# Optimization experiments

Measured on AMD Instinct MI355X. Metric: run time of the kernel, lower is better.

## Reference

```python
import jax, jax.numpy as jnp
import numpy as np

B, T, H, W, D = 8, 16, 64, 64, 256
DK = 128
TOP_K = 4
DECAY = 0.95
TAU = 1.0
EPS = 1e-10


def setup_inputs() -> dict:
    key = jax.random.key(0)
    ks = jax.random.split(key, 6)
    return {
        "query_features": jax.random.normal(ks[0], (B, H, W, D), dtype=jnp.float32),
        "history_buffer": jax.random.normal(ks[1], (B, T, H, W, D), dtype=jnp.float32),
        "W_q": jax.random.normal(ks[2], (D, DK), dtype=jnp.float32) * (1.0 / np.sqrt(D)),
        "W_k": jax.random.normal(ks[3], (D, DK), dtype=jnp.float32) * (1.0 / np.sqrt(D)),
        "W_v": jax.random.normal(ks[4], (D, DK), dtype=jnp.float32) * (1.0 / np.sqrt(D)),
        "W_o": jax.random.normal(ks[5], (DK, D), dtype=jnp.float32) * (1.0 / np.sqrt(DK)),
    }


def reference(query_features, history_buffer, W_q, W_k, W_v, W_o):
    # Projections (Linear, bias=False)
    Q = jnp.einsum("bhwd,dk->bhwk", query_features, W_q)          # [B,H,W,DK]
    K = jnp.einsum("bthwd,dk->bthwk", history_buffer, W_k)        # [B,T,H,W,DK]
    V = jnp.einsum("bthwd,dk->bthwk", history_buffer, W_v)        # [B,T,H,W,DK]

    # Per-pixel temporal scores over T history steps
    scores = jnp.einsum("bhwk,bthwk->bhwt", Q, K) / jnp.sqrt(jnp.float32(DK))  # [B,H,W,T]

    # Top-K gating over the time axis (top_k < T)
    _, topk_idx = jax.lax.top_k(scores, TOP_K)                    # [B,H,W,K]
    mask = jax.nn.one_hot(topk_idx, T, dtype=scores.dtype).sum(axis=-2) > 0  # [B,H,W,T]
    scores = jnp.where(mask, scores, -jnp.inf)

    # Log-decay bias: decay_rate ** (T - t)
    t = jnp.arange(T, dtype=jnp.float32)
    decay_bias = jnp.log(jnp.float32(DECAY) ** (T - t) + EPS)     # [T]
    scores = scores + decay_bias

    attn = jax.nn.softmax(scores / TAU, axis=-1)                  # [B,H,W,T]

    out = jnp.einsum("bhwt,bthwk->bhwk", attn, V)                 # [B,H,W,DK]
    out = jnp.einsum("bhwk,kd->bhwd", out, W_o)                   # [B,H,W,D]
    return out
```

## Files before the change

### kernel.cpp

```cpp
#include <hip/hip_runtime.h>
#include <math.h>


typedef __attribute__((ext_vector_type(8))) short bf16x8;
typedef __attribute__((ext_vector_type(4))) float f32x4;

__device__ inline unsigned short f2bf(float f) {
  union { float f; unsigned u; } v; v.f = f;
  unsigned r = (v.u + 0x7FFF + ((v.u >> 16) & 1)) >> 16;
  return (unsigned short)r;
}
__device__ inline float bf2f(unsigned short h) {
  union { unsigned u; float f; } v; v.u = ((unsigned)h) << 16;
  return v.f;
}
__device__ inline float4 ldnt(const float4* p) {
  f32x4 t = __builtin_nontemporal_load((const f32x4*)p);
  return make_float4(t[0], t[1], t[2], t[3]);
}

__global__ __launch_bounds__(256) void precompute_weights(
    const float* __restrict__ Wq, const float* __restrict__ Wk,
    const float* __restrict__ Wv, const float* __restrict__ Wo,
    unsigned short* __restrict__ M1A, unsigned short* __restrict__ M1B,
    unsigned short* __restrict__ M1C, unsigned short* __restrict__ M2F) {
  __shared__ float rowbuf[128];
  int bid = blockIdx.x, tid = threadIdx.x;
  if (bid < 256) {
    int d = bid;
    if (tid < 128) rowbuf[tid] = Wq[d * 128 + tid];
    __syncthreads();
    const float4* Wk4 = (const float4*)Wk;
    const float4* rb4 = (const float4*)rowbuf;
    float acc = 0.f;
#pragma unroll 8
    for (int k4 = 0; k4 < 32; ++k4) {
      float4 a = rb4[k4];
      float4 b = Wk4[tid * 32 + k4];
      acc = fmaf(a.x, b.x, acc); acc = fmaf(a.y, b.y, acc);
      acc = fmaf(a.z, b.z, acc); acc = fmaf(a.w, b.w, acc);
    }
    int c = tid;
    int ct = c >> 4, kt = d >> 5, lh = (d >> 3) & 3, i = d & 7, lm = c & 15;
    size_t idx = (size_t)(((ct * 8 + kt) * 64 + lh * 16 + lm) * 8 + i);
    unsigned short h0 = f2bf(acc);
    float r1 = acc - bf2f(h0);
    unsigned short h1 = f2bf(r1);
    float r2 = r1 - bf2f(h1);
    M1A[idx] = h0;
    M1B[idx] = h1;
    M1C[idx] = f2bf(r2);
  } else {
    int k = bid - 256;
    if (tid < 128) rowbuf[tid] = Wv[k * 128 + tid];
    __syncthreads();
    float acc = 0.f;
#pragma unroll 8
    for (int kk = 0; kk < 128; ++kk)
      acc = fmaf(rowbuf[kk], Wo[kk * 256 + tid], acc);
    int c = tid;
    int ct = c >> 4, kt = k >> 5, lh = (k >> 3) & 3, i = k & 7, lm = c & 15;
    M2F[(size_t)(((ct * 8 + kt) * 64 + lh * 16 + lm) * 8 + i)] = f2bf(acc);
  }
}

__global__ __launch_bounds__(256, 2) void fused_all(
    const float* __restrict__ query, const float* __restrict__ hist,
    const unsigned short* __restrict__ M1A,
    const unsigned short* __restrict__ M1B,
    const unsigned short* __restrict__ M1C,
    const unsigned short* __restrict__ M2F, float* __restrict__ OUT) {
  __shared__ float As[64][260];
  int tid = threadIdx.x;
  int l = tid & 63;
  int w = tid >> 6;
  int pix0 = blockIdx.x * 64;
  int rot = blockIdx.x & 15;
  int lm = l & 15, lh = l >> 4;

  const float4* H4 = (const float4*)hist;
  int b = pix0 >> 12;
  int off0 = pix0 & 4095;
  size_t hblk = ((size_t)b * 16 * 4096 + off0) * 64 + l;
  int t_mine = l & 15;
  int gbase = l & 48;

  float4 hA[16], hB[16];
  {
    int row0 = w + 4 * rot;
#pragma unroll
    for (int t = 0; t < 16; ++t)
      hA[t] = ldnt(&H4[hblk + (size_t)row0 * 64 + (size_t)t * 262144]);
  }

  {
    const float4* Qb4 = (const float4*)(query + (size_t)pix0 * 256);
    for (int i = tid; i < 4096; i += 256) {
      float4 v = ldnt(&Qb4[i]);
      *(float4*)&As[i >> 6][(i & 63) * 4] = v;
    }
    __syncthreads();

    const bf16x8* BA = (const bf16x8*)M1A;
    const bf16x8* BB = (const bf16x8*)M1B;
    const bf16x8* BC = (const bf16x8*)M1C;
    f32x4 qacc[16];
#pragma unroll
    for (int i = 0; i < 16; ++i) qacc[i] = (f32x4){0.f, 0.f, 0.f, 0.f};
#pragma unroll
    for (int kt = 0; kt < 8; ++kt) {
      bf16x8 qa[4], qb[4], qc[4];
#pragma unroll
      for (int rt = 0; rt < 4; ++rt) {
        const float* ap = &As[rt * 16 + lm][kt * 32 + lh * 8];
        float4 a0 = *(const float4*)ap;
        float4 a1 = *(const float4*)(ap + 4);
        float av[8] = {a0.x, a0.y, a0.z, a0.w, a1.x, a1.y, a1.z, a1.w};
#pragma unroll
        for (int e = 0; e < 8; ++e) {
          unsigned short h0 = f2bf(av[e]);
          float r1 = av[e] - bf2f(h0);
          unsigned short h1 = f2bf(r1);
          float r2 = r1 - bf2f(h1);
          qa[rt][e] = (short)h0;
          qb[rt][e] = (short)h1;
          qc[rt][e] = (short)f2bf(r2);
        }
      }
#pragma unroll
      for (int cc = 0; cc < 4; ++cc) {
        int ct = w * 4 + cc;
        bf16x8 ba = BA[(ct * 8 + kt) * 64 + l];
        bf16x8 bb = BB[(ct * 8 + kt) * 64 + l];
        bf16x8 bc = BC[(ct * 8 + kt) * 64 + l];
#pragma unroll
        for (int rt = 0; rt < 4; ++rt) {
          f32x4 a = qacc[rt * 4 + cc];
          a = __builtin_amdgcn_mfma_f32_16x16x32_bf16(qa[rt], ba, a, 0, 0, 0);
          a = __builtin_amdgcn_mfma_f32_16x16x32_bf16(qa[rt], bb, a, 0, 0, 0);
          a = __builtin_amdgcn_mfma_f32_16x16x32_bf16(qb[rt], ba, a, 0, 0, 0);
          a = __builtin_amdgcn_mfma_f32_16x16x32_bf16(qa[rt], bc, a, 0, 0, 0);
          a = __builtin_amdgcn_mfma_f32_16x16x32_bf16(qb[rt], bb, a, 0, 0, 0);
          a = __builtin_amdgcn_mfma_f32_16x16x32_bf16(qc[rt], ba, a, 0, 0, 0);
          a = __builtin_amdgcn_mfma_f32_16x16x32_bf16(qb[rt], bc, a, 0, 0, 0);
          a = __builtin_amdgcn_mfma_f32_16x16x32_bf16(qc[rt], bb, a, 0, 0, 0);
          qacc[rt * 4 + cc] = a;
        }
      }
    }
    __syncthreads();
#pragma unroll
    for (int rt = 0; rt < 4; ++rt)
#pragma unroll
      for (int cc = 0; cc < 4; ++cc)
#pragma unroll
        for (int j = 0; j < 4; ++j)
          As[rt * 16 + lh * 4 + j][w * 64 + cc * 16 + lm] =
              qacc[rt * 4 + cc][j];
    __syncthreads();
  }

#define ATTN_STEP(HC, HN, I, DOPRE)                                         \
  {                                                                         \
    int row = w + 4 * (((I) + rot) & 15);                                   \
    if (DOPRE) {           \
      int nrow = w + 4 * (((I) + 1 + rot) & 15);                            \
      size_t nb = hblk + (size_t)nrow * 64;                                 \
      _Pragma("unroll") for (int t = 0; t < 16; ++t)                        \
          HN[t] = ldnt(&H4[nb + (size_t)t * 262144]);                       \
    }                                                                       \
    float4 q = *(const float4*)&As[row][4 * l];                             \
    float part[16];                                                         \
    _Pragma("unroll") for (int t = 0; t < 16; ++t) {                        \
      float s = HC[t].x * q.x;                                              \
      s = fmaf(HC[t].y, q.y, s);                                            \
      s = fmaf(HC[t].z, q.z, s);                                            \
      s = fmaf(HC[t].w, q.w, s);                                            \
      part[t] = s;                                                          \
    }                                                                       \
    _Pragma("unroll") for (int st = 0; st < 4; ++st) {                      \
      bool hi = (l >> st) & 1;                                              \
      int nt = 8 >> st;                                                     \
      _Pragma("unroll") for (int i = 0; i < nt; ++i) {                      \
        float mine = hi ? part[2 * i + 1] : part[2 * i];                    \
        float oth = hi ? part[2 * i] : part[2 * i + 1];                     \
        part[i] = mine + __shfl_xor(oth, 1 << st);                          \
      }                                                                     \
    }                                                                       \
    float v = part[0];                                                      \
    v += __shfl_xor(v, 16);                                                 \
    v += __shfl_xor(v, 32);                                                 \
    float sc = v * 0.08838834764831845f;         \
    int rank = 0;              \
    _Pragma("unroll") for (int k = 1; k < 16; ++k) {                        \
      int ot = (t_mine + k) & 15;                                           \
      float o = __shfl(sc, gbase | ot);                                     \
      rank += (o > sc) || (o == sc && ot < t_mine);                         \
    }                                                                       \
    bool chosen = rank < 4;                                                 \
    float earg = sc + (float)(16 - t_mine) * -0.05129329438755058f;         \
    float ex = chosen ? expf(earg) : 0.0f;                                  \
    float Z = ex;                                                           \
    Z += __shfl_xor(Z, 1);                                                  \
    Z += __shfl_xor(Z, 2);                                                  \
    Z += __shfl_xor(Z, 4);                                                  \
    Z += __shfl_xor(Z, 8);                                                  \
    float attn = ex / Z;                                                    \
    float4 hb = make_float4(0.f, 0.f, 0.f, 0.f);                            \
    _Pragma("unroll") for (int t = 0; t < 16; ++t) {                        \
      float a = __shfl(attn, gbase | t);  \
      if (a != 0.0f) {                                                      \
        hb.x = fmaf(a, HC[t].x, hb.x);                                      \
        hb.y = fmaf(a, HC[t].y, hb.y);                                      \
        hb.z = fmaf(a, HC[t].z, hb.z);                                      \
        hb.w = fmaf(a, HC[t].w, hb.w);                                      \
      }                                                                     \
    }                                                                       \
    *(float4*)&As[row][4 * l] = hb;   \
  }

  for (int it2 = 0; it2 < 8; ++it2) {
    ATTN_STEP(hA, hB, 2 * it2, true);
    ATTN_STEP(hB, hA, 2 * it2 + 1, it2 < 7);
  }
#undef ATTN_STEP

  {
    const bf16x8* B8 = (const bf16x8*)M2F;
    f32x4 acc[16];
#pragma unroll
    for (int ct = 0; ct < 16; ++ct) acc[ct] = (f32x4){0.f, 0.f, 0.f, 0.f};
#pragma unroll
    for (int kt = 0; kt < 8; ++kt) {
      const float* ap = &As[w + 4 * lm][kt * 32 + lh * 8];
      float4 a0 = *(const float4*)ap;
      float4 a1 = *(const float4*)(ap + 4);
      bf16x8 afrag;
      afrag[0] = (short)f2bf(a0.x); afrag[1] = (short)f2bf(a0.y);
      afrag[2] = (short)f2bf(a0.z); afrag[3] = (short)f2bf(a0.w);
      afrag[4] = (short)f2bf(a1.x); afrag[5] = (short)f2bf(a1.y);
      afrag[6] = (short)f2bf(a1.z); afrag[7] = (short)f2bf(a1.w);
#pragma unroll
      for (int ct = 0; ct < 16; ++ct) {
        bf16x8 bfrag = B8[(ct * 8 + kt) * 64 + l];
        acc[ct] = __builtin_amdgcn_mfma_f32_16x16x32_bf16(afrag, bfrag,
                                                          acc[ct], 0, 0, 0);
      }
    }
    float* outp = OUT + (size_t)pix0 * 256;
#pragma unroll
    for (int ct = 0; ct < 16; ++ct) {
#pragma unroll
      for (int j = 0; j < 4; ++j)
        __builtin_nontemporal_store(
            acc[ct][j],
            &outp[(size_t)(w + 4 * (lh * 4 + j)) * 256 + ct * 16 + lm]);
    }
  }
}

extern "C" void kernel_launch(void* const* d_in, const int* in_sizes, int n_in,
                              void* d_out, int out_size, void* d_ws,
                              size_t ws_size, hipStream_t stream) {
  const float* query = (const float*)d_in[0];
  const float* hist = (const float*)d_in[1];
  const float* Wq = (const float*)d_in[2];
  const float* Wk = (const float*)d_in[3];
  const float* Wv = (const float*)d_in[4];
  const float* Wo = (const float*)d_in[5];
  float* out = (float*)d_out;

  unsigned short* wsu = (unsigned short*)d_ws;
  unsigned short* M1A = wsu;
  unsigned short* M1B = wsu + 65536;
  unsigned short* M1C = wsu + 131072;
  unsigned short* M2F = wsu + 196608;

  precompute_weights<<<512, 256, 0, stream>>>(Wq, Wk, Wv, Wo, M1A, M1B, M1C,
                                              M2F);
  fused_all<<<512, 256, 0, stream>>>(query, hist, M1A, M1B, M1C, M2F, out);
}
```

Measured before the change: 143.0 us.

## Split attention into score pass and sparse top-k gather of history rows

Restructures the per-pixel attention. Each warp now streams history by time step, reducing full dot products into a shared scores table, then runs top-k and softmax from shared memory. It then gathers only the four selected history rows per pixel to form the weighted sum. Selected rows are re-read from global memory (likely L2 hits) instead of holding all 16 time steps in registers. This lowers register pressure and the masked FMA work, at the cost of a second gather pass, more shuffles per score, and plain stores replacing nontemporal output stores.

```diff
diff --git a/kernel.cpp b/kernel.cpp
--- a/kernel.cpp
+++ b/kernel.cpp
@@ -71,27 +71,22 @@
     const unsigned short* __restrict__ M1C,
     const unsigned short* __restrict__ M2F, float* __restrict__ OUT) {
   __shared__ float As[64][260];
+  __shared__ float scoresS[64][17];
+  __shared__ float attnW[64][4];
+  __shared__ int attnT[64][4];
   int tid = threadIdx.x;
   int l = tid & 63;
   int w = tid >> 6;
   int pix0 = blockIdx.x * 64;
-  int rot = blockIdx.x & 15;
+  int r0 = w * 16;
   int lm = l & 15, lh = l >> 4;
 
   const float4* H4 = (const float4*)hist;
   int b = pix0 >> 12;
   int off0 = pix0 & 4095;
-  size_t hblk = ((size_t)b * 16 * 4096 + off0) * 64 + l;
+  int bT = b * 16;
   int t_mine = l & 15;
   int gbase = l & 48;
-
-  float4 hA[16], hB[16];
-  {
-    int row0 = w + 4 * rot;
-#pragma unroll
-    for (int t = 0; t < 16; ++t)
-      hA[t] = ldnt(&H4[hblk + (size_t)row0 * 64 + (size_t)t * 262144]);
-  }
 
   {
     const float4* Qb4 = (const float4*)(query + (size_t)pix0 * 256);
@@ -160,70 +155,116 @@
     __syncthreads();
   }
 
-#define ATTN_STEP(HC, HN, I, DOPRE)                                         \
+#define B1A(T) (((size_t)(bT + (T)) * 4096 + off0) * 64 + l)
+#define STEP1A(HC, HN, G, CT, NB, NG, DOPRE)                                \
   {                                                                         \
-    int row = w + 4 * (((I) + rot) & 15);                                   \
-    if (DOPRE) {           \
-      int nrow = w + 4 * (((I) + 1 + rot) & 15);                            \
-      size_t nb = hblk + (size_t)nrow * 64;                                 \
-      _Pragma("unroll") for (int t = 0; t < 16; ++t)                        \
-          HN[t] = ldnt(&H4[nb + (size_t)t * 262144]);                       \
+    if (DOPRE) {                                                            \
+      _Pragma("unroll") for (int j = 0; j < 16; ++j)                        \
+          HN[j] = ldnt(&H4[(NB) + (size_t)((NG)*16 + j) * 64]);             \
     }                                                                       \
-    float4 q = *(const float4*)&As[row][4 * l];                             \
-    float part[16];                                                         \
-    _Pragma("unroll") for (int t = 0; t < 16; ++t) {                        \
-      float s = HC[t].x * q.x;                                              \
-      s = fmaf(HC[t].y, q.y, s);                                            \
-      s = fmaf(HC[t].z, q.z, s);                                            \
-      s = fmaf(HC[t].w, q.w, s);                                            \
-      part[t] = s;                                                          \
+    _Pragma("unroll") for (int j = 0; j < 16; ++j) {                        \
+      int px = (G)*16 + j;                                                  \
+      float4 q = *(const float4*)&As[px][4 * l];                            \
+      float s = HC[j].x * q.x;                                              \
+      s = fmaf(HC[j].y, q.y, s);                                            \
+      s = fmaf(HC[j].z, q.z, s);                                            \
+      s = fmaf(HC[j].w, q.w, s);                                            \
+      s += __shfl_xor(s, 1);                                                \
+      s += __shfl_xor(s, 2);                                                \
+      s += __shfl_xor(s, 4);                                                \
+      s += __shfl_xor(s, 8);                                                \
+      s += __shfl_xor(s, 16);                                               \
+      s += __shfl_xor(s, 32);                                               \
+      if (l == 0) scoresS[px][(CT)] = s * 0.08838834764831845f;             \
     }                                                                       \
-    _Pragma("unroll") for (int st = 0; st < 4; ++st) {                      \
-      bool hi = (l >> st) & 1;                                              \
-      int nt = 8 >> st;                                                     \
-      _Pragma("unroll") for (int i = 0; i < nt; ++i) {                      \
-        float mine = hi ? part[2 * i + 1] : part[2 * i];                    \
-        float oth = hi ? part[2 * i] : part[2 * i + 1];                     \
-        part[i] = mine + __shfl_xor(oth, 1 << st);                          \
-      }                                                                     \
-    }                                                                       \
-    float v = part[0];                                                      \
-    v += __shfl_xor(v, 16);                                                 \
-    v += __shfl_xor(v, 32);                                                 \
-    float sc = v * 0.08838834764831845f;         \
-    int rank = 0;              \
-    _Pragma("unroll") for (int k = 1; k < 16; ++k) {                        \
-      int ot = (t_mine + k) & 15;                                           \
-      float o = __shfl(sc, gbase | ot);                                     \
-      rank += (o > sc) || (o == sc && ot < t_mine);                         \
-    }                                                                       \
-    bool chosen = rank < 4;                                                 \
-    float earg = sc + (float)(16 - t_mine) * -0.05129329438755058f;         \
-    float ex = chosen ? expf(earg) : 0.0f;                                  \
-    float Z = ex;                                                           \
-    Z += __shfl_xor(Z, 1);                                                  \
-    Z += __shfl_xor(Z, 2);                                                  \
-    Z += __shfl_xor(Z, 4);                                                  \
-    Z += __shfl_xor(Z, 8);                                                  \
-    float attn = ex / Z;                                                    \
-    float4 hb = make_float4(0.f, 0.f, 0.f, 0.f);                            \
-    _Pragma("unroll") for (int t = 0; t < 16; ++t) {                        \
-      float a = __shfl(attn, gbase | t);  \
-      if (a != 0.0f) {                                                      \
-        hb.x = fmaf(a, HC[t].x, hb.x);                                      \
-        hb.y = fmaf(a, HC[t].y, hb.y);                                      \
-        hb.z = fmaf(a, HC[t].z, hb.z);                                      \
-        hb.w = fmaf(a, HC[t].w, hb.w);                                      \
-      }                                                                     \
-    }                                                                       \
-    *(float4*)&As[row][4 * l] = hb;   \
-  }
-
-  for (int it2 = 0; it2 < 8; ++it2) {
-    ATTN_STEP(hA, hB, 2 * it2, true);
-    ATTN_STEP(hB, hA, 2 * it2 + 1, it2 < 7);
-  }
-#undef ATTN_STEP
+  }
+
+  {
+    float4 hA[16], hB[16];
+#pragma unroll
+    for (int j = 0; j < 16; ++j) hA[j] = ldnt(&H4[B1A(w) + (size_t)j * 64]);
+    STEP1A(hA, hB, 0, w, B1A(w), 1, 1)
+    STEP1A(hB, hA, 1, w, B1A(w), 2, 1)
+    STEP1A(hA, hB, 2, w, B1A(w), 3, 1)
+    STEP1A(hB, hA, 3, w, B1A(w + 4), 0, 1)
+    STEP1A(hA, hB, 0, w + 4, B1A(w + 4), 1, 1)
+    STEP1A(hB, hA, 1, w + 4, B1A(w + 4), 2, 1)
+    STEP1A(hA, hB, 2, w + 4, B1A(w + 4), 3, 1)
+    STEP1A(hB, hA, 3, w + 4, B1A(w + 8), 0, 1)
+    STEP1A(hA, hB, 0, w + 8, B1A(w + 8), 1, 1)
+    STEP1A(hB, hA, 1, w + 8, B1A(w + 8), 2, 1)
+    STEP1A(hA, hB, 2, w + 8, B1A(w + 8), 3, 1)
+    STEP1A(hB, hA, 3, w + 8, B1A(w + 12), 0, 1)
+    STEP1A(hA, hB, 0, w + 12, B1A(w + 12), 1, 1)
+    STEP1A(hB, hA, 1, w + 12, B1A(w + 12), 2, 1)
+    STEP1A(hA, hB, 2, w + 12, B1A(w + 12), 3, 1)
+    STEP1A(hB, hA, 3, w + 12, (size_t)0, 0, 0)
+  }
+#undef STEP1A
+  __syncthreads();
+
+#pragma unroll
+  for (int i = 0; i < 4; ++i) {
+    int p = r0 + 4 * i + (l >> 4);
+    float sc = scoresS[p][t_mine];
+    int rank = 0;
+#pragma unroll
+    for (int k = 1; k < 16; ++k) {
+      int ot = (t_mine + k) & 15;
+      float o = __shfl(sc, gbase | ot);
+      rank += (o > sc) || (o == sc && ot < t_mine);
+    }
+    bool chosen = rank < 4;
+    float earg = sc + (float)(16 - t_mine) * -0.05129329438755058f;
+    float ex = chosen ? expf(earg) : 0.0f;
+    float Z = ex;
+    Z += __shfl_xor(Z, 1);
+    Z += __shfl_xor(Z, 2);
+    Z += __shfl_xor(Z, 4);
+    Z += __shfl_xor(Z, 8);
+    unsigned long long bal = __ballot(chosen);
+    int before = __popcll(bal & ((1ull << l) - 1) & (0xFFFFull << gbase));
+    if (chosen) {
+      attnW[p][before] = ex / Z;
+      attnT[p][before] = t_mine;
+    }
+  }
+
+  for (int i = 0; i < 16; i += 4) {
+    int p0 = r0 + i;
+    float aW[4][4];
+    int aT[4][4];
+#pragma unroll
+    for (int u = 0; u < 4; ++u)
+#pragma unroll
+      for (int j = 0; j < 4; ++j) {
+        aW[u][j] = attnW[p0 + u][j];
+        aT[u][j] = attnT[p0 + u][j];
+      }
+    float4 hv[4][4];
+#pragma unroll
+    for (int u = 0; u < 4; ++u)
+#pragma unroll
+      for (int j = 0; j < 4; ++j)
+        hv[u][j] =
+            H4[((size_t)(bT + aT[u][j]) * 4096 + off0 + p0 + u) * 64 + l];
+#pragma unroll
+    for (int u = 0; u < 4; ++u) {
+      float4 acc;
+      acc.x = aW[u][0] * hv[u][0].x;
+      acc.y = aW[u][0] * hv[u][0].y;
+      acc.z = aW[u][0] * hv[u][0].z;
+      acc.w = aW[u][0] * hv[u][0].w;
+#pragma unroll
+      for (int j = 1; j < 4; ++j) {
+        acc.x = fmaf(aW[u][j], hv[u][j].x, acc.x);
+        acc.y = fmaf(aW[u][j], hv[u][j].y, acc.y);
+        acc.z = fmaf(aW[u][j], hv[u][j].z, acc.z);
+        acc.w = fmaf(aW[u][j], hv[u][j].w, acc.w);
+      }
+      *(float4*)&As[p0 + u][4 * l] = acc;
+    }
+  }
 
   {
     const bf16x8* B8 = (const bf16x8*)M2F;
@@ -232,7 +273,7 @@
     for (int ct = 0; ct < 16; ++ct) acc[ct] = (f32x4){0.f, 0.f, 0.f, 0.f};
 #pragma unroll
     for (int kt = 0; kt < 8; ++kt) {
-      const float* ap = &As[w + 4 * lm][kt * 32 + lh * 8];
+      const float* ap = &As[r0 + lm][kt * 32 + lh * 8];
       float4 a0 = *(const float4*)ap;
       float4 a1 = *(const float4*)(ap + 4);
       bf16x8 afrag;
@@ -252,9 +293,7 @@
     for (int ct = 0; ct < 16; ++ct) {
 #pragma unroll
       for (int j = 0; j < 4; ++j)
-        __builtin_nontemporal_store(
-            acc[ct][j],
-            &outp[(size_t)(w + 4 * (lh * 4 + j)) * 256 + ct * 16 + lm]);
+        outp[(size_t)(r0 + lh * 4 + j) * 256 + ct * 16 + lm] = acc[ct][j];
     }
   }
 }
```

After: 163.8 us. 1.14x slower.
